# Kernel optimization log

Hardware: AMD Instinct MI355X
Metric: run time of the kernel (lower is better)

Reference implementation:

```python
import jax, jax.numpy as jnp
import numpy as np

GROUP = 32  # hadamard_group_size == MXFP4 block size
FP4_GRID = np.array([0.0, 0.5, 1.0, 1.5, 2.0, 3.0, 4.0, 6.0], dtype=np.float32)  # e2m1 magnitudes
FP4_MID = np.array([0.25, 0.75, 1.25, 1.75, 2.5, 3.5, 5.0], dtype=np.float32)    # RTN midpoints


def _hadamard(n):
    # Sylvester construction, normalized so H is orthonormal (matches hadamard(n)*n**-0.5)
    H = np.array([[1.0]], dtype=np.float64)
    while H.shape[0] < n:
        H = np.block([[H, H], [H, -H]])
    return (H / np.sqrt(n)).astype(np.float32)


def _pseudo_quant_mxfp4(t, H, gs):
    """Hadamard-rotate per group of 32, then MXFP4 (e2m1 + power-of-two block scale)
    quant-dequant with abs_max scaling and a global scale. STE through the rounding."""
    shp = t.shape
    rot = t.reshape(-1, GROUP) @ H                      # [n_groups, 32] rotated space
    v = jax.lax.stop_gradient(rot) * gs
    absmax = jnp.max(jnp.abs(v), axis=-1, keepdims=True)
    # E8M0 power-of-two shared scale so that absmax/scale <= 6 (max e2m1 value)
    scale = jnp.exp2(jnp.ceil(jnp.log2(absmax / 6.0 + 1e-30)))
    scale = jnp.where(absmax > 0, scale, 1.0)
    u = v / scale
    grid = jnp.asarray(FP4_GRID)
    mid = jnp.asarray(FP4_MID)
    q = jnp.sign(u) * grid[jnp.searchsorted(mid, jnp.abs(u))]  # round-to-nearest e2m1
    dq = q * scale / gs
    out = rot + jax.lax.stop_gradient(dq - rot)         # straight-through estimator
    return out.reshape(shp)


def setup_inputs() -> dict:
    key = jax.random.key(0)
    kx, kw, kb = jax.random.split(key, 3)
    B, S, K, N = 4, 2048, 4096, 4096
    x = jax.random.normal(kx, (B, S, K), jnp.float32)
    weight = jax.random.normal(kw, (N, K), jnp.float32) * (K ** -0.5)
    bias = jax.random.normal(kb, (N,), jnp.float32)
    H = jnp.asarray(_hadamard(GROUP))
    weight_global_scale = jnp.array([3.0], jnp.float32)  # abs_max method
    act_global_scale = jnp.array([3.0], jnp.float32)
    return {"x": x, "weight": weight, "bias": bias, "hadamard_matrix": H,
            "weight_global_scale": weight_global_scale, "act_global_scale": act_global_scale}


def reference(x, weight, bias, hadamard_matrix, weight_global_scale, act_global_scale):
    x_dq = _pseudo_quant_mxfp4(x, hadamard_matrix, act_global_scale[0])
    w_dq = _pseudo_quant_mxfp4(weight, hadamard_matrix, weight_global_scale[0])
    # both operands stay in the rotated space; per-group Hadamard is orthogonal so
    # x_rot @ w_rot^T == x @ w^T up to quantization error (QuTLASS semantics)
    return jnp.einsum('bsk,nk->bsn', x_dq, w_dq) + bias
```

## Files before the change

### kernel.cpp

```cpp
#include <hip/hip_runtime.h>
#include <hip/hip_bf16.h>

typedef int   i32x4  __attribute__((ext_vector_type(4)));
typedef int   i32x8  __attribute__((ext_vector_type(8)));
typedef float f32x16 __attribute__((ext_vector_type(16)));

__device__ inline void gload_lds16(const void* g, void* l) {
  __builtin_amdgcn_global_load_lds((const __attribute__((address_space(1))) void*)g,
                                   (__attribute__((address_space(3))) void*)l, 16, 0, 0);
}
__device__ inline void gload_lds4(const void* g, void* l) {
  __builtin_amdgcn_global_load_lds((const __attribute__((address_space(1))) void*)g,
                                   (__attribute__((address_space(3))) void*)l, 4, 0, 0);
}
__device__ inline i32x8 pad8(i32x4 v) {
  i32x8 r;
  r[0] = v[0]; r[1] = v[1]; r[2] = v[2]; r[3] = v[3];
  r[4] = 0; r[5] = 0; r[6] = 0; r[7] = 0;
  return r;
}

__global__ __launch_bounds__(256) void quant_pack_fp4(const float* __restrict__ in,
                                                      unsigned char* __restrict__ outq,
                                                      unsigned char* __restrict__ outsc,
                                                      const float* __restrict__ gs_ptr,
                                                      int n_groups, int rows, int kg) {
  int g = blockIdx.x * 256 + threadIdx.x;
  if (g >= n_groups) return;
  const float gs = gs_ptr[0];
  int r = g / kg, j = g - r * kg;

  float t[32];
  const float4* p4 = (const float4*)(in + (size_t)g * 32);
#pragma unroll
  for (int i = 0; i < 8; ++i) {
    float4 v4 = p4[i];
    t[4 * i + 0] = v4.x; t[4 * i + 1] = v4.y;
    t[4 * i + 2] = v4.z; t[4 * i + 3] = v4.w;
  }
#pragma unroll
  for (int s = 0; s < 5; ++s) {
    const int hh = 1 << s;
#pragma unroll
    for (int i = 0; i < 32; ++i) {
      if ((i & hh) == 0) {
        float a = t[i], b = t[i + hh];
        t[i] = a + b;
        t[i + hh] = a - b;
      }
    }
  }

  const float c = 0.17677669529663687f;
  float v[32];
  float am = 0.0f;
#pragma unroll
  for (int i = 0; i < 32; ++i) {
    float vi = (t[i] * c) * gs;
    v[i] = vi;
    am = fmaxf(am, fabsf(vi));
  }

  float a6 = am / 6.0f;
  int ex;
  float mant = frexpf(a6, &ex);
  int e = (mant == 0.5f) ? ex - 1 : ex;
  if (e < -127) e = -127;
  if (e > 127) e = 127;
  float inv_s = ldexpf(1.0f, -e);

  unsigned int dw[4] = {0u, 0u, 0u, 0u};
#pragma unroll
  for (int i = 0; i < 32; ++i) {
    float u = v[i] * inv_s;
    float au = fabsf(u);
    int idx = (au > 0.25f) + (au > 0.75f) + (au > 1.25f) + (au > 1.75f)
            + (au > 2.5f) + (au > 3.5f) + (au > 5.0f);
    int code = idx | ((u < 0.0f) ? 8 : 0);
    dw[i >> 3] |= (unsigned)code << ((i & 7) * 4);
  }
  i32x4 packed;
  packed[0] = (int)dw[0]; packed[1] = (int)dw[1];
  packed[2] = (int)dw[2]; packed[3] = (int)dw[3];
  *(i32x4*)(outq + (size_t)r * ((size_t)kg * 16) + (size_t)j * 16) = packed;

  int s = j >> 3, j0 = j & 7;
  int p = ((j0 & 1) << 2) | (j0 >> 1);
  outsc[((size_t)s * rows + r) * 8 + p] = (unsigned char)(e + 127);
}


#define STAGE(mb, kt, h, ldsHalf) do {                                               \
    const unsigned char* _s = (mb) + (size_t)((h)*64 + (w << 3) + (l >> 3)) * KB2    \
                      + (size_t)(kt) * 128 + (size_t)csw * 16;                       \
    gload_lds16(_s, (unsigned char*)(ldsHalf) + (w << 10));                          \
    gload_lds16(_s + ((size_t)KB2 << 5), (unsigned char*)(ldsHalf) + (w << 10) + 4096); \
  } while (0)

#define STAGE_ASC(kt, bf) gload_lds4(AscG + ((size_t)(kt) * M + brow) * 8 + (tid << 2), \
                                     (unsigned char*)&asc[bf][0] + (w << 8))
#define STAGE_BSC(kt, bf) gload_lds4(BscG + ((size_t)(kt) * N + bcol) * 8 + (tid << 2), \
                                     (unsigned char*)&bsc[bf][0] + (w << 8))

#define LOADB(bf) do {                                                               \
    const unsigned char* _bb = &lds[bf][1][0][0];                                    \
    _Pragma("unroll")                                                                \
    for (int nt = 0; nt < 2; ++nt) {                                                 \
      int row = wn * 64 + nt * 32 + (l & 31);                                        \
      int xr = row & 7;                                                              \
      _Pragma("unroll")                                                              \
      for (int kk = 0; kk < 4; ++kk)                                                 \
        bfr[nt][kk] = *(const i32x4*)(_bb + row * 128 + (((kk * 2 + h) ^ xr) << 4)); \
      sb[nt] = *(const int*)((const unsigned char*)&bsc[bf][0] + row * 8 + h * 4);   \
    } } while (0)

#define LOADA(bf, mt) do {                                                           \
    const unsigned char* _ab = &lds[bf][0][0][0];                                    \
    int row = wm * 64 + (mt) * 32 + (l & 31);                                        \
    int xr = row & 7;                                                                \
    _Pragma("unroll")                                                                \
    for (int kk = 0; kk < 4; ++kk)                                                   \
      af[kk] = *(const i32x4*)(_ab + row * 128 + (((kk * 2 + h) ^ xr) << 4));        \
    sa = *(const int*)((const unsigned char*)&asc[bf][0] + row * 8 + h * 4);         \
  } while (0)

#define MF1(mt, nt, kk)                                                              \
  acc[mt][nt] = __builtin_amdgcn_mfma_scale_f32_32x32x64_f8f6f4(                     \
      pad8(af[kk]), pad8(bfr[nt][kk]), acc[mt][nt], 4, 4, kk, sa, kk, sb[nt]);

#define MFMAQ(mt) do {                                                               \
    __builtin_amdgcn_s_setprio(1);                                                   \
    MF1(mt, 0, 0) MF1(mt, 1, 0) MF1(mt, 0, 1) MF1(mt, 1, 1)                          \
    MF1(mt, 0, 2) MF1(mt, 1, 2) MF1(mt, 0, 3) MF1(mt, 1, 3)                          \
    __builtin_amdgcn_s_setprio(0);                                                   \
  } while (0)

#define MIDSYNC() do { __builtin_amdgcn_s_barrier();                                 \
    asm volatile("s_waitcnt lgkmcnt(0)" ::: "memory");                               \
    __builtin_amdgcn_sched_barrier(0); } while (0)

#define ENDP() __builtin_amdgcn_s_barrier()
#define VM5()  asm volatile("s_waitcnt vmcnt(5)" ::: "memory")

__global__ __launch_bounds__(256, 2) void gemm128_fp4(const unsigned char* __restrict__ Aq,
                                                      const unsigned char* __restrict__ Bq,
                                                      const unsigned char* __restrict__ AscG,
                                                      const unsigned char* __restrict__ BscG,
                                                      float* __restrict__ C,
                                                      const float* __restrict__ bias,
                                                      const float* __restrict__ gsx,
                                                      const float* __restrict__ gsw,
                                                      int M, int N, int K) {
  __shared__ __align__(16) unsigned char lds[2][2][2][8192];
  __shared__ __align__(16) unsigned char asc[2][1024];
  __shared__ __align__(16) unsigned char bsc[2][1024];

  const int tid = threadIdx.x;
  const int w = tid >> 6, l = tid & 63;
  const int wm = w >> 1, wn = w & 1;
  const int h = l >> 5;
  const int csw = (l & 7) ^ (l >> 3);
  const int KB2 = K >> 1;

  const int nwg = gridDim.x;
  int bid = blockIdx.x;
  if ((nwg & 7) == 0) bid = (bid & 7) * (nwg >> 3) + (bid >> 3);
  const int ntn = N / 128;
  const size_t brow = (size_t)(bid / ntn) * 128;
  const size_t bcol = (size_t)(bid % ntn) * 128;

  const unsigned char* Ab = Aq + brow * (size_t)KB2;
  const unsigned char* Bb = Bq + bcol * (size_t)KB2;

  f32x16 acc[2][2];
#pragma unroll
  for (int m = 0; m < 2; ++m)
#pragma unroll
    for (int n = 0; n < 2; ++n)
#pragma unroll
      for (int r = 0; r < 16; ++r) acc[m][n][r] = 0.0f;

  i32x4 af[4], bfr[2][4];
  int sa, sb[2];

  const int nkt = K / 256;

  STAGE(Ab, 0, 0, &lds[0][0][0][0]); STAGE(Ab, 0, 1, &lds[0][0][1][0]); STAGE_ASC(0, 0);
  STAGE(Bb, 0, 0, &lds[0][1][0][0]); STAGE(Bb, 0, 1, &lds[0][1][1][0]); STAGE_BSC(0, 0);
  STAGE(Bb, 1, 0, &lds[1][1][0][0]); STAGE(Bb, 1, 1, &lds[1][1][1][0]); STAGE_BSC(1, 1);
  VM5();
  __builtin_amdgcn_s_barrier();

  for (int t = 0; t < nkt; ++t) {
    const int p = t & 1;
    const int ta = (t + 1 < nkt) ? t + 1 : nkt - 1;
    const int tb = (t + 2 < nkt) ? t + 2 : nkt - 1;

    LOADB(p); LOADA(p, 0);
    STAGE(Ab, ta, 0, &lds[1 - p][0][0][0]);
    STAGE(Ab, ta, 1, &lds[1 - p][0][1][0]);
    STAGE_ASC(ta, 1 - p);
    MIDSYNC(); MFMAQ(0); ENDP();

    LOADA(p, 1);
    STAGE(Bb, tb, 0, &lds[p][1][0][0]);
    STAGE(Bb, tb, 1, &lds[p][1][1][0]);
    STAGE_BSC(tb, p);
    MIDSYNC(); MFMAQ(1); VM5(); ENDP();
  }

  const float inv = 1.0f / (gsx[0] * gsw[0]);
#pragma unroll
  for (int nt = 0; nt < 2; ++nt) {
    const int col = (int)bcol + wn * 64 + nt * 32 + (l & 31);
    const float bv = bias[col];
#pragma unroll
    for (int mt = 0; mt < 2; ++mt) {
      const size_t rbase = brow + (size_t)(wm * 64 + mt * 32 + 4 * h);
#pragma unroll
      for (int r = 0; r < 16; ++r) {
        const size_t row = rbase + (r & 3) + 8 * (r >> 2);
        C[row * (size_t)N + col] = acc[mt][nt][r] * inv + bv;
      }
    }
  }
}

extern "C" void kernel_launch(void* const* d_in, const int* in_sizes, int n_in,
                              void* d_out, int out_size, void* d_ws, size_t ws_size,
                              hipStream_t stream) {
  const float* x    = (const float*)d_in[0];
  const float* wgt  = (const float*)d_in[1];
  const float* bias = (const float*)d_in[2];
  const float* wgs  = (const float*)d_in[4];
  const float* ags  = (const float*)d_in[5];

  const int N = in_sizes[2];
  const int K = in_sizes[1] / N;
  const int M = in_sizes[0] / K;
  const int kg = K / 32;

  unsigned char* aq  = (unsigned char*)d_ws;
  unsigned char* bq  = aq + (size_t)M * (K / 2);
  unsigned char* asc = bq + (size_t)N * (K / 2);
  unsigned char* bsc = asc + (size_t)M * kg;

  const int xg = in_sizes[0] / 32;
  const int wg = in_sizes[1] / 32;
  quant_pack_fp4<<<dim3((xg + 255) / 256), dim3(256), 0, stream>>>(x, aq, asc, ags, xg, M, kg);
  quant_pack_fp4<<<dim3((wg + 255) / 256), dim3(256), 0, stream>>>(wgt, bq, bsc, wgs, wg, N, kg);

  dim3 grid((M / 128) * (N / 128));
  gemm128_fp4<<<grid, dim3(256), 0, stream>>>(aq, bq, asc, bsc, (float*)d_out, bias,
                                              ags, wgs, M, N, K);
}
```

Measured before the change: 160.4 us.

## Deepen A prefetch to two tiles, reorder staging, add L2-friendly tile swizzle

The GEMM main loop now prefetches both A and B two K-tiles ahead. Global-to-LDS stage loads are issued after the mid-iteration barrier, so they overlap the MFMA quarter, and the wait threshold is raised to vmcnt(10). The block-to-tile mapping becomes a grouped swizzle of 8x8 column groups per XCD chunk, meant to improve L2 reuse. The quant kernel also gathers per-block scale bytes in shared memory and writes them as 4-byte words instead of scattered single bytes. It drops the out-of-range guard, which assumes the group count divides evenly into blocks.

```diff
diff --git a/kernel.cpp b/kernel.cpp
--- a/kernel.cpp
+++ b/kernel.cpp
@@ -26,7 +26,6 @@
                                                       const float* __restrict__ gs_ptr,
                                                       int n_groups, int rows, int kg) {
   int g = blockIdx.x * 256 + threadIdx.x;
-  if (g >= n_groups) return;
   const float gs = gs_ptr[0];
   int r = g / kg, j = g - r * kg;
 
@@ -86,7 +85,19 @@
 
   int s = j >> 3, j0 = j & 7;
   int p = ((j0 & 1) << 2) | (j0 >> 1);
-  outsc[((size_t)s * rows + r) * 8 + p] = (unsigned char)(e + 127);
+  if (kg == 128) {
+    __shared__ unsigned char sl[256];
+    sl[(s << 4) | ((r & 1) << 3) | p] = (unsigned char)(e + 127);
+    __syncthreads();
+    if (threadIdx.x < 64) {
+      int si = threadIdx.x >> 2, wd = threadIdx.x & 3;
+      unsigned int vv = *(const unsigned int*)&sl[(si << 4) | (wd << 2)];
+      size_t r0 = (size_t)blockIdx.x * 2;
+      *(unsigned int*)(outsc + ((size_t)si * rows + r0) * 8 + (wd << 2)) = vv;
+    }
+  } else {
+    outsc[((size_t)s * rows + r) * 8 + p] = (unsigned char)(e + 127);
+  }
 }
 
 
@@ -140,7 +151,7 @@
     __builtin_amdgcn_sched_barrier(0); } while (0)
 
 #define ENDP() __builtin_amdgcn_s_barrier()
-#define VM5()  asm volatile("s_waitcnt vmcnt(5)" ::: "memory")
+#define VM10() asm volatile("s_waitcnt vmcnt(10)" ::: "memory")
 
 __global__ __launch_bounds__(256, 2) void gemm128_fp4(const unsigned char* __restrict__ Aq,
                                                       const unsigned char* __restrict__ Bq,
@@ -162,12 +173,28 @@
   const int csw = (l & 7) ^ (l >> 3);
   const int KB2 = K >> 1;
 
+  const int ntn = N >> 7;
   const int nwg = gridDim.x;
-  int bid = blockIdx.x;
-  if ((nwg & 7) == 0) bid = (bid & 7) * (nwg >> 3) + (bid >> 3);
-  const int ntn = N / 128;
-  const size_t brow = (size_t)(bid / ntn) * 128;
-  const size_t bcol = (size_t)(bid % ntn) * 128;
+  int r_t, c_t;
+  {
+    int bid = blockIdx.x;
+    if ((nwg & 7) == 0) {
+      int x = bid & 7, o = bid >> 3, cpx = nwg >> 3;
+      int rpx = cpx / ntn;
+      if ((ntn & 7) == 0 && rpx > 0 && (cpx % ntn) == 0) {
+        int g8 = o & 7, rr = (o >> 3) % rpx, ss = o / (8 * rpx);
+        r_t = x * rpx + rr;
+        c_t = ss * 8 + g8;
+      } else {
+        int lin = x * cpx + o;
+        r_t = lin / ntn; c_t = lin % ntn;
+      }
+    } else {
+      r_t = bid / ntn; c_t = bid % ntn;
+    }
+  }
+  const size_t brow = (size_t)r_t * 128;
+  const size_t bcol = (size_t)c_t * 128;
 
   const unsigned char* Ab = Aq + brow * (size_t)KB2;
   const unsigned char* Bb = Bq + bcol * (size_t)KB2;
@@ -188,25 +215,30 @@
   STAGE(Ab, 0, 0, &lds[0][0][0][0]); STAGE(Ab, 0, 1, &lds[0][0][1][0]); STAGE_ASC(0, 0);
   STAGE(Bb, 0, 0, &lds[0][1][0][0]); STAGE(Bb, 0, 1, &lds[0][1][1][0]); STAGE_BSC(0, 0);
   STAGE(Bb, 1, 0, &lds[1][1][0][0]); STAGE(Bb, 1, 1, &lds[1][1][1][0]); STAGE_BSC(1, 1);
-  VM5();
+  STAGE(Ab, 1, 0, &lds[1][0][0][0]); STAGE(Ab, 1, 1, &lds[1][0][1][0]); STAGE_ASC(1, 1);
+  VM10();
   __builtin_amdgcn_s_barrier();
 
   for (int t = 0; t < nkt; ++t) {
     const int p = t & 1;
-    const int ta = (t + 1 < nkt) ? t + 1 : nkt - 1;
-    const int tb = (t + 2 < nkt) ? t + 2 : nkt - 1;
+    const int t2 = (t + 2 < nkt) ? t + 2 : nkt - 1;
 
     LOADB(p); LOADA(p, 0);
-    STAGE(Ab, ta, 0, &lds[1 - p][0][0][0]);
-    STAGE(Ab, ta, 1, &lds[1 - p][0][1][0]);
-    STAGE_ASC(ta, 1 - p);
-    MIDSYNC(); MFMAQ(0); ENDP();
+    MIDSYNC();
+    STAGE(Bb, t2, 0, &lds[p][1][0][0]);
+    STAGE(Bb, t2, 1, &lds[p][1][1][0]);
+    STAGE_BSC(t2, p);
+    MFMAQ(0);
+    ENDP();
 
     LOADA(p, 1);
-    STAGE(Bb, tb, 0, &lds[p][1][0][0]);
-    STAGE(Bb, tb, 1, &lds[p][1][1][0]);
-    STAGE_BSC(tb, p);
-    MIDSYNC(); MFMAQ(1); VM5(); ENDP();
+    MIDSYNC();
+    STAGE(Ab, t2, 0, &lds[p][0][0][0]);
+    STAGE(Ab, t2, 1, &lds[p][0][1][0]);
+    STAGE_ASC(t2, p);
+    MFMAQ(1);
+    VM10();
+    ENDP();
   }
 
   const float inv = 1.0f / (gsx[0] * gsw[0]);
```

Result: faster. 155.9 us (-2.9%).
